# Optimization experiments

Measured on AMD Instinct MI355X. Metric: run time of the kernel, lower is better.

Reference implementation:

```python
import jax, jax.numpy as jnp
import numpy as np

N = 50000
E = 800000
D_IN = 128
D_OUT = 64


def setup_inputs() -> dict:
    key = jax.random.key(0)
    ks = jax.random.split(key, 8)
    x = jax.random.normal(ks[0], (N, D_IN), dtype=jnp.float32)
    edge_index = jax.random.randint(ks[1], (2, E), 0, N, dtype=jnp.int64)
    s = 1.0 / np.sqrt(D_IN)
    # PyG SAGEConv: lin_l (applied to aggregated neighbors, has bias), lin_r (root, no bias)
    w1_l = jax.random.uniform(ks[2], (D_IN, D_IN), jnp.float32, -s, s)
    b1 = jnp.zeros((D_IN,), jnp.float32)
    w1_r = jax.random.uniform(ks[3], (D_IN, D_IN), jnp.float32, -s, s)
    w2_l = jax.random.uniform(ks[4], (D_IN, D_OUT), jnp.float32, -s, s)
    b2 = jnp.zeros((D_OUT,), jnp.float32)
    w2_r = jax.random.uniform(ks[5], (D_IN, D_OUT), jnp.float32, -s, s)
    return {"x": x, "edge_index": edge_index, "w1_l": w1_l, "b1": b1,
            "w1_r": w1_r, "w2_l": w2_l, "b2": b2, "w2_r": w2_r}


def _sage_conv(x, src, dst, w_l, b_l, w_r):
    # mean-aggregate source features at destination nodes
    msg_sum = jax.ops.segment_sum(x[src], dst, num_segments=N)  # [N, d]
    cnt = jax.ops.segment_sum(jnp.ones((src.shape[0],), x.dtype), dst, num_segments=N)
    mean = msg_sum / jnp.maximum(cnt, 1.0)[:, None]
    out = mean @ w_l + b_l + x @ w_r
    # L2 normalize (normalize=True)
    norm = jnp.linalg.norm(out, axis=-1, keepdims=True)
    return out / jnp.maximum(norm, 1e-12)


def reference(x, edge_index, w1_l, b1, w1_r, w2_l, b2, w2_r):
    src, dst = edge_index[0], edge_index[1]
    h = _sage_conv(x, src, dst, w1_l, b1, w1_r)
    h = _sage_conv(h, src, dst, w2_l, b2, w2_r)
    return h
```

## Files before the change

### kernel.cpp

```cpp
#include <hip/hip_runtime.h>
#include <math.h>

#define NN 50000
#define EE 800000
#define NB 196
#define CAP 6144

typedef __attribute__((ext_vector_type(8))) short bf16x8;
typedef __attribute__((ext_vector_type(16))) float f32x16;
typedef __attribute__((ext_vector_type(4))) unsigned short us4;

__device__ inline unsigned short bf16_rne(float f) {
    union { float f; unsigned u; } a; a.f = f;
    unsigned u = a.u;
    u += 0x7fff + ((u >> 16) & 1);
    return (unsigned short)(u >> 16);
}
__device__ inline float bf16_lo(unsigned v) {
    union { unsigned u; float f; } a; a.u = v << 16;
    return a.f;
}
__device__ inline float bf16_hi(unsigned v) {
    union { unsigned u; float f; } a; a.u = v & 0xffff0000u;
    return a.f;
}

__global__ void prep_all_kernel(const float* __restrict__ w1l, const float* __restrict__ w1r,
                                const float* __restrict__ w2l, const float* __restrict__ w2r,
                                unsigned short* __restrict__ wt1, unsigned short* __restrict__ wt2,
                                unsigned short* __restrict__ y1pad, unsigned short* __restrict__ y2pad,
                                int* __restrict__ bcur) {
    int idx = blockIdx.x * 256 + threadIdx.x;
    if (idx < 32768) {
        int n = idx >> 7, k = idx & 127;
        float v = (n < 128) ? w1l[(size_t)k * 128 + n] : w1r[(size_t)k * 128 + (n - 128)];
        wt1[idx] = bf16_rne(v);
    } else if (idx < 49152) {
        int j = idx - 32768;
        int n = j >> 7, k = j & 127;
        float v = (n < 64) ? w2l[(size_t)k * 64 + n] : w2r[(size_t)k * 64 + (n - 64)];
        wt2[j] = bf16_rne(v);
    } else {
        int j = idx - 49152;
        if (j < 128) y1pad[j] = 0;
        else if (j < 192) y2pad[j - 128] = 0;
        else if (j < 192 + NB) bcur[j - 192] = 0;
    }
}

__global__ __launch_bounds__(1024) void bin_kernel(
        const int* __restrict__ src, const int* __restrict__ dst,
        int* __restrict__ gcur, int* __restrict__ rec, int E) {
    __shared__ int hist[NB];
    __shared__ int cur[NB];
    const int t = threadIdx.x;
    const int per = (E + gridDim.x - 1) / gridDim.x;
    const int lo = blockIdx.x * per;
    const int hi = min(lo + per, E);

    for (int i = t; i < NB; i += 1024) hist[i] = 0;
    __syncthreads();
    for (int e = lo + t; e < hi; e += 1024)
        atomicAdd(&hist[dst[e] >> 8], 1);
    __syncthreads();
    for (int i = t; i < NB; i += 1024)
        cur[i] = atomicAdd(&gcur[i], hist[i]);
    __syncthreads();
    for (int e = lo + t; e < hi; e += 1024) {
        int d = dst[e], s = src[e];
        int cb = d >> 8;
        int p = atomicAdd(&cur[cb], 1);
        if (p < CAP) rec[(size_t)cb * CAP + p] = ((d & 255) << 16) | s;
    }
}

__global__ __launch_bounds__(256) void place_kernel(
        const int* __restrict__ rec, const int* __restrict__ bcur,
        int* __restrict__ rowoff, unsigned short* __restrict__ csr, int n) {
    __shared__ int bscan[256];
    __shared__ int cnt[256];
    __shared__ int cur[256];
    __shared__ unsigned short sorted[CAP];
    const int cb = blockIdx.x, t = threadIdx.x;

    bscan[t] = (t < NB) ? bcur[t] : 0;
    __syncthreads();
    for (int ofs = 1; ofs < 256; ofs <<= 1) {
        int v = bscan[t];
        int a = (t >= ofs) ? bscan[t - ofs] : 0;
        __syncthreads();
        bscan[t] = v + a;
        __syncthreads();
    }
    const int base = (cb == 0) ? 0 : bscan[cb - 1];

    int m = bcur[cb]; if (m > CAP) m = CAP;
    const int* r = rec + (size_t)cb * CAP;

    cnt[t] = 0;
    __syncthreads();
    for (int i = t; i < m; i += 256) atomicAdd(&cnt[r[i] >> 16], 1);
    __syncthreads();
    int orig = cnt[t];
    for (int ofs = 1; ofs < 256; ofs <<= 1) {
        int v = cnt[t];
        int a = (t >= ofs) ? cnt[t - ofs] : 0;
        __syncthreads();
        cnt[t] = v + a;
        __syncthreads();
    }
    int excl = cnt[t] - orig;
    int node = cb * 256 + t;
    if (node < n) rowoff[node] = base + excl;
    if (node == n - 1) rowoff[n] = base + cnt[t];
    cur[t] = excl;
    __syncthreads();
    for (int i = t; i < m; i += 256) {
        int rr = r[i];
        int pos = atomicAdd(&cur[rr >> 16], 1);
        sorted[pos] = (unsigned short)(rr & 0xffff);
    }
    __syncthreads();
    for (int i = t; i < m; i += 256) csr[base + i] = sorted[i];
}

template <int CO, bool BF16IN>
__global__ __launch_bounds__(256) void transform_mfma_kernel(
        const void* __restrict__ xin, const unsigned short* __restrict__ wt,
        const float* __restrict__ bias, unsigned short* __restrict__ ybuf,
        unsigned short* __restrict__ rbuf, int n) {
    constexpr int HALF = CO / 2;
    constexpr int LDW = 136;
    __shared__ unsigned short Xs[64][LDW];
    __shared__ unsigned short Ws[64][LDW];

    const int t = threadIdx.x;
    const int node0 = blockIdx.x * 64;
    const int gy = blockIdx.y;

    if (BF16IN) {
        const unsigned short* xb = (const unsigned short*)xin;
        for (int e = t; e < 64 * 16; e += 256) {
            int nd = e >> 4, c8 = e & 15;
            int node = node0 + nd;
            int4 v = (node < n) ? ((const int4*)(xb + (size_t)node * 128))[c8]
                                : make_int4(0, 0, 0, 0);
            *(int4*)&Xs[nd][c8 * 8] = v;
        }
    } else {
        const float* xf = (const float*)xin;
        for (int e = t; e < 64 * 32; e += 256) {
            int nd = e >> 5, c4 = e & 31;
            int node = node0 + nd;
            float4 v = (node < n) ? ((const float4*)xf)[(size_t)node * 32 + c4]
                                  : make_float4(0.f, 0.f, 0.f, 0.f);
            us4 p;
            p.x = bf16_rne(v.x); p.y = bf16_rne(v.y); p.z = bf16_rne(v.z); p.w = bf16_rne(v.w);
            *(us4*)&Xs[nd][c4 * 4] = p;
        }
    }
    for (int e = t; e < 64 * 16; e += 256) {
        int nd = e >> 4, c8 = e & 15;
        int4 v = ((const int4*)(wt + ((size_t)(gy * 64 + nd)) * 128))[c8];
        *(int4*)&Ws[nd][c8 * 8] = v;
    }
    __syncthreads();

    const int lane = t & 63, wave = t >> 6;
    const int wm = (wave & 1) * 32, wn = (wave >> 1) * 32;
    const int ml = wm + (lane & 31);
    const int nl = wn + (lane & 31);
    const int koff = (lane >> 5) * 8;

    f32x16 acc;
#pragma unroll
    for (int r = 0; r < 16; r++) acc[r] = 0.f;

#pragma unroll
    for (int kk = 0; kk < 8; kk++) {
        bf16x8 a = *(const bf16x8*)&Xs[ml][kk * 16 + koff];
        bf16x8 b = *(const bf16x8*)&Ws[nl][kk * 16 + koff];
        acc = __builtin_amdgcn_mfma_f32_32x32x16_bf16(a, b, acc, 0, 0, 0);
    }

    const int col = gy * 64 + wn + (lane & 31);
    if (col < HALF) {
#pragma unroll
        for (int r = 0; r < 16; r++) {
            int row = (r & 3) + 8 * (r >> 2) + 4 * (lane >> 5);
            int node = node0 + wm + row;
            if (node < n) ybuf[(size_t)node * HALF + col] = bf16_rne(acc[r]);
        }
    } else {
        const float bj = bias[col - HALF];
#pragma unroll
        for (int r = 0; r < 16; r++) {
            int row = (r & 3) + 8 * (r >> 2) + 4 * (lane >> 5);
            int node = node0 + wm + row;
            if (node < n) rbuf[(size_t)node * HALF + (col - HALF)] = bf16_rne(acc[r] + bj);
        }
    }
}

__global__ __launch_bounds__(256) void gather128_kernel(
        const unsigned short* __restrict__ y, const unsigned short* __restrict__ rrb,
        const int* __restrict__ rowoff, const unsigned short* __restrict__ csr,
        unsigned short* __restrict__ out, int n) {
    const int gi = threadIdx.x >> 4;
    const int q  = threadIdx.x & 15;
    const int node = blockIdx.x * 16 + gi;
    if (node >= n) return;

    const int off = rowoff[node];
    const int end = rowoff[node + 1];
    const int deg = end - off;

    float acc[8];
#pragma unroll
    for (int j = 0; j < 8; j++) acc[j] = 0.f;

    for (int k0 = 0; k0 < deg; k0 += 8) {
        int idx[8];
#pragma unroll
        for (int j = 0; j < 8; j++) {
            int kk = off + k0 + j;
            idx[j] = (kk < end) ? (int)csr[kk] : n;
        }
        uint4 v[8];
#pragma unroll
        for (int j = 0; j < 8; j++)
            v[j] = *(const uint4*)(y + (size_t)idx[j] * 128 + q * 8);
#pragma unroll
        for (int j = 0; j < 8; j++) {
            const unsigned* u = (const unsigned*)&v[j];
#pragma unroll
            for (int i = 0; i < 4; i++) {
                acc[2 * i]     += bf16_lo(u[i]);
                acc[2 * i + 1] += bf16_hi(u[i]);
            }
        }
    }
    const float im = 1.0f / fmaxf((float)deg, 1.0f);
    uint4 rv = *(const uint4*)(rrb + (size_t)node * 128 + q * 8);
    const unsigned* ru = (const unsigned*)&rv;
    float v[8];
    float ss = 0.f;
#pragma unroll
    for (int i = 0; i < 4; i++) {
        v[2 * i]     = acc[2 * i] * im     + bf16_lo(ru[i]);
        v[2 * i + 1] = acc[2 * i + 1] * im + bf16_hi(ru[i]);
    }
#pragma unroll
    for (int j = 0; j < 8; j++) ss += v[j] * v[j];
#pragma unroll
    for (int m = 8; m >= 1; m >>= 1) ss += __shfl_xor(ss, m, 64);
    const float rn = 1.0f / fmaxf(sqrtf(ss), 1e-12f);
    uint4 pk;
    unsigned* pu = (unsigned*)&pk;
#pragma unroll
    for (int i = 0; i < 4; i++)
        pu[i] = (unsigned)bf16_rne(v[2 * i] * rn) |
                ((unsigned)bf16_rne(v[2 * i + 1] * rn) << 16);
    *(uint4*)(out + (size_t)node * 128 + q * 8) = pk;
}

__global__ __launch_bounds__(256) void gather64_kernel(
        const unsigned short* __restrict__ y, const unsigned short* __restrict__ rrb,
        const int* __restrict__ rowoff, const unsigned short* __restrict__ csr,
        float* __restrict__ out, int n) {
    const int gi = threadIdx.x >> 3;
    const int q  = threadIdx.x & 7;
    const int node = blockIdx.x * 32 + gi;
    if (node >= n) return;

    const int off = rowoff[node];
    const int end = rowoff[node + 1];
    const int deg = end - off;

    float acc[8];
#pragma unroll
    for (int j = 0; j < 8; j++) acc[j] = 0.f;

    for (int k0 = 0; k0 < deg; k0 += 8) {
        int idx[8];
#pragma unroll
        for (int j = 0; j < 8; j++) {
            int kk = off + k0 + j;
            idx[j] = (kk < end) ? (int)csr[kk] : n;
        }
        uint4 v[8];
#pragma unroll
        for (int j = 0; j < 8; j++)
            v[j] = *(const uint4*)(y + (size_t)idx[j] * 64 + q * 8);
#pragma unroll
        for (int j = 0; j < 8; j++) {
            const unsigned* u = (const unsigned*)&v[j];
#pragma unroll
            for (int i = 0; i < 4; i++) {
                acc[2 * i]     += bf16_lo(u[i]);
                acc[2 * i + 1] += bf16_hi(u[i]);
            }
        }
    }
    const float im = 1.0f / fmaxf((float)deg, 1.0f);
    uint4 rv = *(const uint4*)(rrb + (size_t)node * 64 + q * 8);
    const unsigned* ru = (const unsigned*)&rv;
    float v[8];
    float ss = 0.f;
#pragma unroll
    for (int i = 0; i < 4; i++) {
        v[2 * i]     = acc[2 * i] * im     + bf16_lo(ru[i]);
        v[2 * i + 1] = acc[2 * i + 1] * im + bf16_hi(ru[i]);
    }
#pragma unroll
    for (int j = 0; j < 8; j++) ss += v[j] * v[j];
#pragma unroll
    for (int m = 4; m >= 1; m >>= 1) ss += __shfl_xor(ss, m, 64);
    const float rn = 1.0f / fmaxf(sqrtf(ss), 1e-12f);
    float4 o0 = make_float4(v[0] * rn, v[1] * rn, v[2] * rn, v[3] * rn);
    float4 o1 = make_float4(v[4] * rn, v[5] * rn, v[6] * rn, v[7] * rn);
    *(float4*)(out + (size_t)node * 64 + q * 8) = o0;
    *(float4*)(out + (size_t)node * 64 + q * 8 + 4) = o1;
}

extern "C" void kernel_launch(void* const* d_in, const int* in_sizes, int n_in,
                              void* d_out, int out_size, void* d_ws, size_t ws_size,
                              hipStream_t stream) {
    const float* x   = (const float*)d_in[0];
    const int*   ei  = (const int*)d_in[1];
    const float* w1l = (const float*)d_in[2];
    const float* b1  = (const float*)d_in[3];
    const float* w1r = (const float*)d_in[4];
    const float* w2l = (const float*)d_in[5];
    const float* b2  = (const float*)d_in[6];
    const float* w2r = (const float*)d_in[7];
    float* out = (float*)d_out;

    const int* src = ei;
    const int* dst = ei + EE;

    char* ws = (char*)d_ws;
    auto align = [](size_t v) { return (v + 255) & ~(size_t)255; };
    int*   rowoff = (int*)ws;                 size_t o = align((size_t)(NN + 1) * 4);
    int*   bcur   = (int*)(ws + o);           o += align((size_t)NB * 4);
    int*   rec    = (int*)(ws + o);           o += align((size_t)NB * CAP * 4);
    unsigned short* csr = (unsigned short*)(ws + o); o += align((size_t)EE * 2);
    unsigned short* wt1 = (unsigned short*)(ws + o); o += align((size_t)256 * 128 * 2);
    unsigned short* wt2 = (unsigned short*)(ws + o); o += align((size_t)128 * 128 * 2);
    unsigned short* y1  = (unsigned short*)(ws + o); o += align((size_t)(NN + 1) * 128 * 2);
    unsigned short* r1  = (unsigned short*)(ws + o); o += align((size_t)NN * 128 * 2);
    unsigned short* h1  = (unsigned short*)(ws + o); o += align((size_t)NN * 128 * 2);
    unsigned short* y2  = (unsigned short*)(ws + o); o += align((size_t)(NN + 1) * 64 * 2);
    unsigned short* r2  = (unsigned short*)(ws + o); o += align((size_t)NN * 64 * 2);

    prep_all_kernel<<<194, 256, 0, stream>>>(w1l, w1r, w2l, w2r, wt1, wt2,
                                             y1 + (size_t)NN * 128, y2 + (size_t)NN * 64, bcur);
    bin_kernel<<<256, 1024, 0, stream>>>(src, dst, bcur, rec, EE);
    place_kernel<<<NB, 256, 0, stream>>>(rec, bcur, rowoff, csr, NN);

    transform_mfma_kernel<256, false><<<dim3((NN + 63) / 64, 4), 256, 0, stream>>>(
        x, wt1, b1, y1, r1, NN);
    gather128_kernel<<<(NN + 15) / 16, 256, 0, stream>>>(y1, r1, rowoff, csr, h1, NN);

    transform_mfma_kernel<128, true><<<dim3((NN + 63) / 64, 2), 256, 0, stream>>>(
        h1, wt2, b2, y2, r2, NN);
    gather64_kernel<<<(NN + 31) / 32, 256, 0, stream>>>(y2, r2, rowoff, csr, out, NN);
}
```

Measured before the change: 189.6 us.

## Fuse layer-1 transform with edge binning and layer-2 transform into gather

Merges the layer-1 MFMA transform and the edge binning into one launch, with block ranges split between the two independent jobs so they run concurrently. It also folds the layer-2 linear transform into the layer-1 gather kernel using 16x16x32 MFMA on the normalized rows held in shared memory. This drops the h1 intermediate buffer and two launches. In exchange each gather block reloads the full 128x128 W2 tile into LDS and the kernel uses more shared memory, which may lower occupancy. The node bounds check was removed on the assumption that N divides 16.

```diff
diff --git a/kernel.cpp b/kernel.cpp
--- a/kernel.cpp
+++ b/kernel.cpp
@@ -5,9 +5,12 @@
 #define EE 800000
 #define NB 196
 #define CAP 6144
+#define TB1 3128
+#define NBIN 512
 
 typedef __attribute__((ext_vector_type(8))) short bf16x8;
 typedef __attribute__((ext_vector_type(16))) float f32x16;
+typedef __attribute__((ext_vector_type(4))) float f32x4;
 typedef __attribute__((ext_vector_type(4))) unsigned short us4;
 
 __device__ inline unsigned short bf16_rne(float f) {
@@ -48,29 +51,92 @@
     }
 }
 
-__global__ __launch_bounds__(1024) void bin_kernel(
+__global__ __launch_bounds__(256) void fused_t1_bin_kernel(
+        const float* __restrict__ x, const unsigned short* __restrict__ wt,
+        const float* __restrict__ bias, unsigned short* __restrict__ ybuf,
+        unsigned short* __restrict__ rbuf, int n,
         const int* __restrict__ src, const int* __restrict__ dst,
         int* __restrict__ gcur, int* __restrict__ rec, int E) {
+    __shared__ unsigned short Xs[64][136];
+    __shared__ unsigned short Ws[64][136];
     __shared__ int hist[NB];
     __shared__ int cur[NB];
     const int t = threadIdx.x;
-    const int per = (E + gridDim.x - 1) / gridDim.x;
-    const int lo = blockIdx.x * per;
-    const int hi = min(lo + per, E);
-
-    for (int i = t; i < NB; i += 1024) hist[i] = 0;
-    __syncthreads();
-    for (int e = lo + t; e < hi; e += 1024)
-        atomicAdd(&hist[dst[e] >> 8], 1);
-    __syncthreads();
-    for (int i = t; i < NB; i += 1024)
-        cur[i] = atomicAdd(&gcur[i], hist[i]);
-    __syncthreads();
-    for (int e = lo + t; e < hi; e += 1024) {
-        int d = dst[e], s = src[e];
-        int cb = d >> 8;
-        int p = atomicAdd(&cur[cb], 1);
-        if (p < CAP) rec[(size_t)cb * CAP + p] = ((d & 255) << 16) | s;
+
+    if (blockIdx.x >= TB1) {
+        const int bb = blockIdx.x - TB1;
+        const int per = (E + NBIN - 1) / NBIN;
+        const int lo = bb * per;
+        const int hi = min(lo + per, E);
+        for (int i = t; i < NB; i += 256) hist[i] = 0;
+        __syncthreads();
+        for (int e = lo + t; e < hi; e += 256)
+            atomicAdd(&hist[dst[e] >> 8], 1);
+        __syncthreads();
+        for (int i = t; i < NB; i += 256)
+            cur[i] = atomicAdd(&gcur[i], hist[i]);
+        __syncthreads();
+        for (int e = lo + t; e < hi; e += 256) {
+            int d = dst[e], s = src[e];
+            int cb = d >> 8;
+            int p = atomicAdd(&cur[cb], 1);
+            if (p < CAP) rec[(size_t)cb * CAP + p] = ((d & 255) << 16) | s;
+        }
+        return;
+    }
+
+    constexpr int HALF = 128;
+    const int node0 = (blockIdx.x >> 2) * 64;
+    const int gy = blockIdx.x & 3;
+
+    for (int e = t; e < 64 * 32; e += 256) {
+        int nd = e >> 5, c4 = e & 31;
+        int node = node0 + nd;
+        float4 v = (node < n) ? ((const float4*)x)[(size_t)node * 32 + c4]
+                              : make_float4(0.f, 0.f, 0.f, 0.f);
+        us4 p;
+        p.x = bf16_rne(v.x); p.y = bf16_rne(v.y); p.z = bf16_rne(v.z); p.w = bf16_rne(v.w);
+        *(us4*)&Xs[nd][c4 * 4] = p;
+    }
+    for (int e = t; e < 64 * 16; e += 256) {
+        int nd = e >> 4, c8 = e & 15;
+        int4 v = ((const int4*)(wt + ((size_t)(gy * 64 + nd)) * 128))[c8];
+        *(int4*)&Ws[nd][c8 * 8] = v;
+    }
+    __syncthreads();
+
+    const int lane = t & 63, wave = t >> 6;
+    const int wm = (wave & 1) * 32, wn = (wave >> 1) * 32;
+    const int ml = wm + (lane & 31);
+    const int nl = wn + (lane & 31);
+    const int koff = (lane >> 5) * 8;
+
+    f32x16 acc;
+#pragma unroll
+    for (int r = 0; r < 16; r++) acc[r] = 0.f;
+#pragma unroll
+    for (int kk = 0; kk < 8; kk++) {
+        bf16x8 a = *(const bf16x8*)&Xs[ml][kk * 16 + koff];
+        bf16x8 b = *(const bf16x8*)&Ws[nl][kk * 16 + koff];
+        acc = __builtin_amdgcn_mfma_f32_32x32x16_bf16(a, b, acc, 0, 0, 0);
+    }
+
+    const int col = gy * 64 + wn + (lane & 31);
+    if (col < HALF) {
+#pragma unroll
+        for (int r = 0; r < 16; r++) {
+            int row = (r & 3) + 8 * (r >> 2) + 4 * (lane >> 5);
+            int node = node0 + wm + row;
+            if (node < n) ybuf[(size_t)node * HALF + col] = bf16_rne(acc[r]);
+        }
+    } else {
+        const float bj = bias[col - HALF];
+#pragma unroll
+        for (int r = 0; r < 16; r++) {
+            int row = (r & 3) + 8 * (r >> 2) + 4 * (lane >> 5);
+            int node = node0 + wm + row;
+            if (node < n) rbuf[(size_t)node * HALF + (col - HALF)] = bf16_rne(acc[r] + bj);
+        }
     }
 }
 
@@ -124,92 +190,24 @@
     for (int i = t; i < m; i += 256) csr[base + i] = sorted[i];
 }
 
-template <int CO, bool BF16IN>
-__global__ __launch_bounds__(256) void transform_mfma_kernel(
-        const void* __restrict__ xin, const unsigned short* __restrict__ wt,
-        const float* __restrict__ bias, unsigned short* __restrict__ ybuf,
-        unsigned short* __restrict__ rbuf, int n) {
-    constexpr int HALF = CO / 2;
-    constexpr int LDW = 136;
-    __shared__ unsigned short Xs[64][LDW];
-    __shared__ unsigned short Ws[64][LDW];
-
-    const int t = threadIdx.x;
-    const int node0 = blockIdx.x * 64;
-    const int gy = blockIdx.y;
-
-    if (BF16IN) {
-        const unsigned short* xb = (const unsigned short*)xin;
-        for (int e = t; e < 64 * 16; e += 256) {
-            int nd = e >> 4, c8 = e & 15;
-            int node = node0 + nd;
-            int4 v = (node < n) ? ((const int4*)(xb + (size_t)node * 128))[c8]
-                                : make_int4(0, 0, 0, 0);
-            *(int4*)&Xs[nd][c8 * 8] = v;
-        }
-    } else {
-        const float* xf = (const float*)xin;
-        for (int e = t; e < 64 * 32; e += 256) {
-            int nd = e >> 5, c4 = e & 31;
-            int node = node0 + nd;
-            float4 v = (node < n) ? ((const float4*)xf)[(size_t)node * 32 + c4]
-                                  : make_float4(0.f, 0.f, 0.f, 0.f);
-            us4 p;
-            p.x = bf16_rne(v.x); p.y = bf16_rne(v.y); p.z = bf16_rne(v.z); p.w = bf16_rne(v.w);
-            *(us4*)&Xs[nd][c4 * 4] = p;
-        }
-    }
-    for (int e = t; e < 64 * 16; e += 256) {
-        int nd = e >> 4, c8 = e & 15;
-        int4 v = ((const int4*)(wt + ((size_t)(gy * 64 + nd)) * 128))[c8];
-        *(int4*)&Ws[nd][c8 * 8] = v;
-    }
-    __syncthreads();
-
-    const int lane = t & 63, wave = t >> 6;
-    const int wm = (wave & 1) * 32, wn = (wave >> 1) * 32;
-    const int ml = wm + (lane & 31);
-    const int nl = wn + (lane & 31);
-    const int koff = (lane >> 5) * 8;
-
-    f32x16 acc;
-#pragma unroll
-    for (int r = 0; r < 16; r++) acc[r] = 0.f;
-
-#pragma unroll
-    for (int kk = 0; kk < 8; kk++) {
-        bf16x8 a = *(const bf16x8*)&Xs[ml][kk * 16 + koff];
-        bf16x8 b = *(const bf16x8*)&Ws[nl][kk * 16 + koff];
-        acc = __builtin_amdgcn_mfma_f32_32x32x16_bf16(a, b, acc, 0, 0, 0);
-    }
-
-    const int col = gy * 64 + wn + (lane & 31);
-    if (col < HALF) {
-#pragma unroll
-        for (int r = 0; r < 16; r++) {
-            int row = (r & 3) + 8 * (r >> 2) + 4 * (lane >> 5);
-            int node = node0 + wm + row;
-            if (node < n) ybuf[(size_t)node * HALF + col] = bf16_rne(acc[r]);
-        }
-    } else {
-        const float bj = bias[col - HALF];
-#pragma unroll
-        for (int r = 0; r < 16; r++) {
-            int row = (r & 3) + 8 * (r >> 2) + 4 * (lane >> 5);
-            int node = node0 + wm + row;
-            if (node < n) rbuf[(size_t)node * HALF + (col - HALF)] = bf16_rne(acc[r] + bj);
-        }
-    }
-}
-
-__global__ __launch_bounds__(256) void gather128_kernel(
+__global__ __launch_bounds__(256) void gather_l2_kernel(
         const unsigned short* __restrict__ y, const unsigned short* __restrict__ rrb,
         const int* __restrict__ rowoff, const unsigned short* __restrict__ csr,
-        unsigned short* __restrict__ out, int n) {
-    const int gi = threadIdx.x >> 4;
-    const int q  = threadIdx.x & 15;
+        const unsigned short* __restrict__ wt2, const float* __restrict__ b2,
+        unsigned short* __restrict__ y2, unsigned short* __restrict__ r2, int n) {
+    __shared__ unsigned short Hs[16][136];
+    __shared__ unsigned short Ws[128][136];
+    const int t = threadIdx.x;
+
+    for (int e = t; e < 128 * 16; e += 256) {
+        int nd = e >> 4, c8 = e & 15;
+        int4 v = ((const int4*)(wt2 + (size_t)nd * 128))[c8];
+        *(int4*)&Ws[nd][c8 * 8] = v;
+    }
+
+    const int gi = t >> 4;
+    const int q  = t & 15;
     const int node = blockIdx.x * 16 + gi;
-    if (node >= n) return;
 
     const int off = rowoff[node];
     const int end = rowoff[node + 1];
@@ -255,13 +253,38 @@
 #pragma unroll
     for (int m = 8; m >= 1; m >>= 1) ss += __shfl_xor(ss, m, 64);
     const float rn = 1.0f / fmaxf(sqrtf(ss), 1e-12f);
-    uint4 pk;
-    unsigned* pu = (unsigned*)&pk;
-#pragma unroll
-    for (int i = 0; i < 4; i++)
-        pu[i] = (unsigned)bf16_rne(v[2 * i] * rn) |
-                ((unsigned)bf16_rne(v[2 * i + 1] * rn) << 16);
-    *(uint4*)(out + (size_t)node * 128 + q * 8) = pk;
+    us4 h0, h1v;
+    h0.x = bf16_rne(v[0] * rn); h0.y = bf16_rne(v[1] * rn);
+    h0.z = bf16_rne(v[2] * rn); h0.w = bf16_rne(v[3] * rn);
+    h1v.x = bf16_rne(v[4] * rn); h1v.y = bf16_rne(v[5] * rn);
+    h1v.z = bf16_rne(v[6] * rn); h1v.w = bf16_rne(v[7] * rn);
+    *(us4*)&Hs[gi][q * 8] = h0;
+    *(us4*)&Hs[gi][q * 8 + 4] = h1v;
+    __syncthreads();
+
+    const int lane = t & 63, wave = t >> 6;
+    const int m16 = lane & 15;
+    const int quad = lane >> 4;
+#pragma unroll
+    for (int tile = 0; tile < 2; tile++) {
+        const int c0 = (wave * 2 + tile) * 16;
+        f32x4 c;
+        c[0] = 0.f; c[1] = 0.f; c[2] = 0.f; c[3] = 0.f;
+#pragma unroll
+        for (int kk = 0; kk < 4; kk++) {
+            bf16x8 a = *(const bf16x8*)&Hs[m16][kk * 32 + quad * 8];
+            bf16x8 b = *(const bf16x8*)&Ws[c0 + m16][kk * 32 + quad * 8];
+            c = __builtin_amdgcn_mfma_f32_16x16x32_bf16(a, b, c, 0, 0, 0);
+        }
+        const int col = c0 + m16;
+#pragma unroll
+        for (int r = 0; r < 4; r++) {
+            int row = quad * 4 + r;
+            int nd = blockIdx.x * 16 + row;
+            if (col < 64) y2[(size_t)nd * 64 + col] = bf16_rne(c[r]);
+            else          r2[(size_t)nd * 64 + (col - 64)] = bf16_rne(c[r] + b2[col - 64]);
+        }
+    }
 }
 
 __global__ __launch_bounds__(256) void gather64_kernel(
@@ -349,20 +372,14 @@
     unsigned short* wt2 = (unsigned short*)(ws + o); o += align((size_t)128 * 128 * 2);
     unsigned short* y1  = (unsigned short*)(ws + o); o += align((size_t)(NN + 1) * 128 * 2);
     unsigned short* r1  = (unsigned short*)(ws + o); o += align((size_t)NN * 128 * 2);
-    unsigned short* h1  = (unsigned short*)(ws + o); o += align((size_t)NN * 128 * 2);
     unsigned short* y2  = (unsigned short*)(ws + o); o += align((size_t)(NN + 1) * 64 * 2);
     unsigned short* r2  = (unsigned short*)(ws + o); o += align((size_t)NN * 64 * 2);
 
     prep_all_kernel<<<194, 256, 0, stream>>>(w1l, w1r, w2l, w2r, wt1, wt2,
                                              y1 + (size_t)NN * 128, y2 + (size_t)NN * 64, bcur);
-    bin_kernel<<<256, 1024, 0, stream>>>(src, dst, bcur, rec, EE);
+    fused_t1_bin_kernel<<<TB1 + NBIN, 256, 0, stream>>>(
+        x, wt1, b1, y1, r1, NN, src, dst, bcur, rec, EE);
     place_kernel<<<NB, 256, 0, stream>>>(rec, bcur, rowoff, csr, NN);
-
-    transform_mfma_kernel<256, false><<<dim3((NN + 63) / 64, 4), 256, 0, stream>>>(
-        x, wt1, b1, y1, r1, NN);
-    gather128_kernel<<<(NN + 15) / 16, 256, 0, stream>>>(y1, r1, rowoff, csr, h1, NN);
-
-    transform_mfma_kernel<128, true><<<dim3((NN + 63) / 64, 2), 256, 0, stream>>>(
-        h1, wt2, b2, y2, r2, NN);
+    gather_l2_kernel<<<NN / 16, 256, 0, stream>>>(y1, r1, rowoff, csr, wt2, b2, y2, r2, NN);
     gather64_kernel<<<(NN + 31) / 32, 256, 0, stream>>>(y2, r2, rowoff, csr, out, NN);
 }
```

Result: no change. 188.0 us (-0.8%).
